# Kernel tuning notes

Hardware: AMD Instinct MI355X
Metric: run time of the kernel (lower is better)

## Reference

```python
import jax, jax.numpy as jnp
import numpy as np

B, S, D, H = 2, 2048, 2048, 16
NEG = -1e9


def setup_inputs() -> dict:
    key = jax.random.key(0)
    ks = jax.random.split(key, 5)
    x = jax.random.normal(ks[0], (B, S, D), dtype=jnp.float32)
    # additive causal mask: 0 on/below diagonal, -1e9 above
    causal = jnp.triu(jnp.full((S, S), NEG, dtype=jnp.float32), k=1)
    attn_mask = causal[None, None, :, :]  # [1,1,S,S]
    scale = 0.02
    Wq = jax.random.normal(ks[1], (D, D), dtype=jnp.float32) * scale
    Wk = jax.random.normal(ks[2], (D, D), dtype=jnp.float32) * scale
    Wv = jax.random.normal(ks[3], (D, D), dtype=jnp.float32) * scale
    Wo = jax.random.normal(ks[4], (D, D), dtype=jnp.float32) * scale
    return {"x": x, "attn_mask": attn_mask, "Wq": Wq, "Wk": Wk, "Wv": Wv, "Wo": Wo}


def reference(x, attn_mask, Wq, Wk, Wv, Wo):
    b, s, hidden = x.shape
    d = hidden // H
    # torch nn.Linear: y = x @ W.T (no bias since bias=None)
    q = (x @ Wq.T).reshape(b, s, H, d).transpose(0, 2, 1, 3)  # [b,h,s,d]
    k = (x @ Wk.T).reshape(b, s, H, d).transpose(0, 2, 1, 3)
    v = (x @ Wv.T).reshape(b, s, H, d).transpose(0, 2, 1, 3)
    q = q * (1.0 / float(d) ** 0.5)
    att = jnp.einsum("bhqd,bhkd->bhqk", q, k) + attn_mask  # [b,h,s,s]
    att = jax.nn.softmax(att.astype(jnp.float32), axis=-1).astype(x.dtype)
    y = jnp.einsum("bhqk,bhkd->bhqd", att, v)
    y = y.transpose(0, 2, 1, 3).reshape(b, s, hidden)
    return y @ Wo.T
```

## Files before the change

kernel.cpp:

```cpp
#include <hip/hip_runtime.h>
#include <hip/hip_bf16.h>
#include <cstdint>
#include <cstddef>

typedef __bf16 bf16;
typedef __bf16 bf16x8 __attribute__((ext_vector_type(8)));
typedef __bf16 bf16x4 __attribute__((ext_vector_type(4)));
typedef float f32x4 __attribute__((ext_vector_type(4)));

static constexpr int BATCH = 2;
static constexpr int SEQ = 2048;
static constexpr int DMODEL = 2048;
static constexpr int NH = 16;
static constexpr int HD = 128;
static constexpr int MROWS = BATCH * SEQ;

#define GLOBAL_AS(p) ((const __attribute__((address_space(1))) void*)(p))
#define LDS_AS(p)    ((__attribute__((address_space(3))) void*)(p))

__global__ void cvt5_kernel(const float* __restrict__ x,
                            const float* __restrict__ wq, const float* __restrict__ wk,
                            const float* __restrict__ wv, const float* __restrict__ wo,
                            bf16* __restrict__ dst) {
  const int i = blockIdx.x * blockDim.x + threadIdx.x;
  const float* src;
  int local;
  if (i < 2097152) { src = x; local = i; }
  else {
    const int r = i - 2097152;
    const int w = r >> 20;
    local = r & 1048575;
    src = (w == 0) ? wq : (w == 1) ? wk : (w == 2) ? wv : wo;
  }
  float4 f = reinterpret_cast<const float4*>(src)[local];
  bf16x4 o;
  o.x = (bf16)f.x; o.y = (bf16)f.y; o.z = (bf16)f.z; o.w = (bf16)f.w;
  reinterpret_cast<bf16x4*>(dst)[i] = o;
}

enum { MODE_QKV = 0, MODE_OUT = 1 };

template <int MODE>
__global__ __launch_bounds__(256, 4) void gemm_bt(
    const bf16* __restrict__ A, const bf16* __restrict__ W,
    bf16* __restrict__ Oq, bf16* __restrict__ Ok, bf16* __restrict__ Ov,
    float* __restrict__ Oout) {
  constexpr int Kd = DMODEL;
  __shared__ __align__(16) bf16 As[128][64];
  __shared__ __align__(16) bf16 Bs[128][64];
  const int n0 = blockIdx.x * 128;
  const int m0 = blockIdx.y * 128;
  const int tid = threadIdx.x;
  const int wave = tid >> 6;
  const int lane = tid & 63;
  const int quad = lane >> 4;
  const int l16 = lane & 15;
  const int wm = (wave >> 1) * 64;
  const int wn = (wave & 1) * 64;
  const int srow = lane >> 3;
  const int schunk = ((lane & 7) - srow) & 7;

  f32x4 acc[4][4] = {};
  for (int kt = 0; kt < Kd; kt += 64) {
#pragma unroll
    for (int i = 0; i < 4; i++) {
      const int r = wave * 32 + i * 8;
      __builtin_amdgcn_global_load_lds(
          GLOBAL_AS(&A[(size_t)(m0 + r + srow) * Kd + kt + schunk * 8]),
          LDS_AS(&As[r][0]), 16, 0, 0);
      __builtin_amdgcn_global_load_lds(
          GLOBAL_AS(&W[(size_t)(n0 + r + srow) * Kd + kt + schunk * 8]),
          LDS_AS(&Bs[r][0]), 16, 0, 0);
    }
    __syncthreads();
#pragma unroll
    for (int ks = 0; ks < 2; ks++) {
      const int col = (((ks * 4 + quad + l16) & 7)) * 8;
      bf16x8 af[4], bfr[4];
#pragma unroll
      for (int t = 0; t < 4; t++)
        af[t] = *reinterpret_cast<const bf16x8*>(&As[wm + t * 16 + l16][col]);
#pragma unroll
      for (int t = 0; t < 4; t++)
        bfr[t] = *reinterpret_cast<const bf16x8*>(&Bs[wn + t * 16 + l16][col]);
#pragma unroll
      for (int tm = 0; tm < 4; tm++)
#pragma unroll
        for (int tn = 0; tn < 4; tn++)
          acc[tm][tn] = __builtin_amdgcn_mfma_f32_16x16x32_bf16(af[tm], bfr[tn], acc[tm][tn], 0, 0, 0);
    }
    __syncthreads();
  }
#pragma unroll
  for (int tm = 0; tm < 4; tm++) {
#pragma unroll
    for (int tn = 0; tn < 4; tn++) {
      const int row0 = m0 + wm + tm * 16 + quad * 4;
      if constexpr (MODE == MODE_OUT) {
        const int col = n0 + wn + tn * 16 + l16;
#pragma unroll
        for (int j = 0; j < 4; j++)
          Oout[(size_t)(row0 + j) * DMODEL + col] = acc[tm][tn][j];
      } else {
        const int mat = n0 >> 11;
        const int col = (n0 & 2047) + wn + tn * 16 + l16;
        const int h = col >> 7, dd = col & 127;
        if (mat == 2) {
          const int b = row0 >> 11, s = row0 & 2047;
          bf16x4 pk;
#pragma unroll
          for (int j = 0; j < 4; j++) pk[j] = (bf16)acc[tm][tn][j];
          *reinterpret_cast<bf16x4*>(&Ov[((size_t)(b * NH + h) * HD + dd) * SEQ + s]) = pk;
        } else {
          bf16* O = mat ? Ok : Oq;
          const float scale = mat ? 1.0f : 0.08838834764831845f;
#pragma unroll
          for (int j = 0; j < 4; j++) {
            const int row = row0 + j;
            const int b = row >> 11, s = row & 2047;
            O[((size_t)(b * NH + h) * SEQ + s) * HD + dd] = (bf16)(acc[tm][tn][j] * scale);
          }
        }
      }
    }
  }
}

__global__ __launch_bounds__(256, 2) void attn_kernel(
    const bf16* __restrict__ Q, const bf16* __restrict__ K,
    const bf16* __restrict__ Vt, bf16* __restrict__ Y) {
  const int j = blockIdx.x;
  const int bh = blockIdx.y;
  __shared__ __align__(16) char smem[74752];
  auto Ks0 = (bf16(*)[128])(smem);
  auto Ks1 = (bf16(*)[128])(smem + 16384);
  auto Vt0 = (bf16(*)[64])(smem + 32768);
  auto Vt1 = (bf16(*)[64])(smem + 49152);
  auto Ps  = (bf16(*)[16][72])(smem + 65536);
  const int tid = threadIdx.x;
  const int wave = tid >> 6;
  const int lane = tid & 63;
  const int quad = lane >> 4;
  const int l16 = lane & 15;

  const bf16* Kbh = K + (size_t)bh * SEQ * HD;
  const bf16* Vbh = Vt + (size_t)bh * HD * SEQ;
  const int b = bh >> 4, h = bh & 15;

  const int krow = lane >> 4;
  const int vrow = lane >> 3;
  const int vchunk = ((lane & 7) - vrow) & 7;

  auto stageK = [&](int kt, bf16 (*Kd)[128]) {
#pragma unroll
    for (int i = 0; i < 4; i++) {
      const int rbase = wave * 16 + i * 4;
      const int r = rbase + krow;
      const int c = ((lane & 15) - krow - i * 4) & 15;
      __builtin_amdgcn_global_load_lds(
          GLOBAL_AS(&Kbh[(size_t)(kt + r) * HD + c * 8]), LDS_AS(&Kd[rbase][0]), 16, 0, 0);
    }
  };
  auto stageV = [&](int kt, bf16 (*Vd)[64]) {
#pragma unroll
    for (int i = 0; i < 4; i++) {
      const int rbase = wave * 32 + i * 8;
      const int r = rbase + vrow;
      __builtin_amdgcn_global_load_lds(
          GLOBAL_AS(&Vbh[(size_t)r * SEQ + kt + vchunk * 8]), LDS_AS(&Vd[rbase][0]), 16, 0, 0);
    }
  };

  for (int pass = 0; pass < 2; ++pass) {
    const int qt = pass ? (31 - j) : j;
    const int q0 = qt * 64;
    const int ntiles = qt + 1;

    const bf16* Qw = Q + ((size_t)bh * SEQ + q0 + wave * 16) * HD;
    bf16x8 qf[4];
#pragma unroll
    for (int kk = 0; kk < 4; kk++)
      qf[kk] = *reinterpret_cast<const bf16x8*>(&Qw[(size_t)l16 * HD + kk * 32 + quad * 8]);

    f32x4 oacc[8] = {};
    float m_i = -3.0e38f, l_i = 0.f;

    stageK(0, Ks0);
    stageV(0, Vt0);
    asm volatile("s_waitcnt vmcnt(0)" ::: "memory");
    __builtin_amdgcn_s_barrier();
    __builtin_amdgcn_sched_barrier(0);

    for (int t = 0; t < ntiles; ++t) {
      bf16 (*Ksc)[128] = (t & 1) ? Ks1 : Ks0;
      bf16 (*Vtc)[64]  = (t & 1) ? Vt1 : Vt0;
      if (t + 1 < ntiles) {
        bf16 (*Ksn)[128] = (t & 1) ? Ks0 : Ks1;
        bf16 (*Vtn)[64]  = (t & 1) ? Vt0 : Vt1;
        stageK((t + 1) * 64, Ksn);
        stageV((t + 1) * 64, Vtn);
      }

      f32x4 sacc[4] = {};
#pragma unroll
      for (int kk = 0; kk < 4; kk++) {
        const int kcol = (((kk * 4 + quad + l16) & 15)) * 8;
        bf16x8 ka[4];
#pragma unroll
        for (int mt = 0; mt < 4; mt++)
          ka[mt] = *reinterpret_cast<const bf16x8*>(&Ksc[mt * 16 + l16][kcol]);
#pragma unroll
        for (int mt = 0; mt < 4; mt++)
          sacc[mt] = __builtin_amdgcn_mfma_f32_16x16x32_bf16(ka[mt], qf[kk], sacc[mt], 0, 0, 0);
      }

      const int qg_loc = wave * 16 + l16;
      float mx = -3.0e38f;
      if (t == ntiles - 1) {
#pragma unroll
        for (int mt = 0; mt < 4; mt++)
#pragma unroll
          for (int jj = 0; jj < 4; jj++) {
            const int kg = mt * 16 + quad * 4 + jj;
            float v = (kg <= qg_loc) ? sacc[mt][jj] : -3.0e38f;
            sacc[mt][jj] = v;
            mx = fmaxf(mx, v);
          }
      } else {
#pragma unroll
        for (int mt = 0; mt < 4; mt++)
#pragma unroll
          for (int jj = 0; jj < 4; jj++) mx = fmaxf(mx, sacc[mt][jj]);
      }
      mx = fmaxf(mx, __shfl_xor(mx, 16));
      mx = fmaxf(mx, __shfl_xor(mx, 32));
      const float mnew = fmaxf(m_i, mx);
      const float alpha = __expf(m_i - mnew);
      m_i = mnew;
      float rs = 0.f;
#pragma unroll
      for (int mt = 0; mt < 4; mt++)
#pragma unroll
        for (int jj = 0; jj < 4; jj++) {
          float p = __expf(sacc[mt][jj] - mnew);
          sacc[mt][jj] = p;
          rs += p;
        }
      rs += __shfl_xor(rs, 16);
      rs += __shfl_xor(rs, 32);
      l_i = l_i * alpha + rs;
#pragma unroll
      for (int mt8 = 0; mt8 < 8; mt8++)
#pragma unroll
        for (int jj = 0; jj < 4; jj++) oacc[mt8][jj] *= alpha;

#pragma unroll
      for (int mt = 0; mt < 4; mt++) {
        bf16x4 pk;
#pragma unroll
        for (int jj = 0; jj < 4; jj++) pk[jj] = (bf16)sacc[mt][jj];
        *reinterpret_cast<bf16x4*>(&Ps[wave][l16][mt * 16 + quad * 4]) = pk;
      }

#pragma unroll
      for (int kk2 = 0; kk2 < 2; kk2++) {
        const int vcol = ((kk2 * 4 + quad + l16) & 7) * 8;
        bf16x8 pb = *reinterpret_cast<const bf16x8*>(&Ps[wave][l16][kk2 * 32 + quad * 8]);
#pragma unroll
        for (int mt8 = 0; mt8 < 8; mt8++) {
          bf16x8 av = *reinterpret_cast<const bf16x8*>(&Vtc[mt8 * 16 + l16][vcol]);
          oacc[mt8] = __builtin_amdgcn_mfma_f32_16x16x32_bf16(av, pb, oacc[mt8], 0, 0, 0);
        }
      }

      asm volatile("s_waitcnt vmcnt(0)" ::: "memory");
      __builtin_amdgcn_s_barrier();
      __builtin_amdgcn_sched_barrier(0);
    }

    const float inv = 1.0f / l_i;
    const int qg = q0 + wave * 16 + l16;
#pragma unroll
    for (int mt8 = 0; mt8 < 8; mt8++) {
      bf16x4 pk;
#pragma unroll
      for (int jj = 0; jj < 4; jj++) pk[jj] = (bf16)(oacc[mt8][jj] * inv);
      *reinterpret_cast<bf16x4*>(
          &Y[(size_t)(b * SEQ + qg) * DMODEL + h * HD + mt8 * 16 + quad * 4]) = pk;
    }
  }
}

extern "C" void kernel_launch(void* const* d_in, const int* in_sizes, int n_in,
                              void* d_out, int out_size, void* d_ws, size_t ws_size,
                              hipStream_t stream) {
  const float* x  = (const float*)d_in[0];
  const float* Wq = (const float*)d_in[2];
  const float* Wk = (const float*)d_in[3];
  const float* Wv = (const float*)d_in[4];
  const float* Wo = (const float*)d_in[5];
  float* out = (float*)d_out;

  char* ws = (char*)d_ws;
  bf16* xb  = (bf16*)(ws + 0);
  bf16* Wqb = (bf16*)(ws + 16777216);
  bf16* Wob = (bf16*)(ws + 41943040);
  bf16* Qb  = (bf16*)(ws + 50331648);
  bf16* Kb  = (bf16*)(ws + 67108864);
  bf16* Vtb = (bf16*)(ws + 83886080);
  bf16* Yb  = xb;
  if (ws_size < 100663296) return;

  cvt5_kernel<<<24576, 256, 0, stream>>>(x, Wq, Wk, Wv, Wo, xb);

  gemm_bt<MODE_QKV><<<dim3(48, MROWS / 128), 256, 0, stream>>>(
      xb, Wqb, Qb, Kb, Vtb, nullptr);

  attn_kernel<<<dim3(16, BATCH * NH), 256, 0, stream>>>(Qb, Kb, Vtb, Yb);

  gemm_bt<MODE_OUT><<<dim3(16, MROWS / 128), 256, 0, stream>>>(
      Yb, Wob, nullptr, nullptr, nullptr, out);
}
```

Before: 357.7 us.

## Process two 64-row query subtiles per block sharing staged K/V tiles

Each attention block now owns one 128-row query strip, split into two 64-row subtiles with separate online-softmax state. Every K/V tile staged into LDS is used by both subtiles, which halves global-to-LDS staging and the barriers per unit of work. The old scheme gave each block two 64-row passes (j and 31-j) to balance causal work. The new scheme drops that pairing and instead reverses the strip order for half the batch-heads. The cost is double the accumulator registers and unequal work per block, ranging from 2 to 32 key tiles.

After: 367.9 us. 1.03x slower.

```diff
diff --git a/kernel.cpp b/kernel.cpp
--- a/kernel.cpp
+++ b/kernel.cpp
@@ -129,8 +129,11 @@
 __global__ __launch_bounds__(256, 2) void attn_kernel(
     const bf16* __restrict__ Q, const bf16* __restrict__ K,
     const bf16* __restrict__ Vt, bf16* __restrict__ Y) {
-  const int j = blockIdx.x;
+  const int xblk = blockIdx.x;
   const int bh = blockIdx.y;
+  const int st = (bh & 16) ? (15 - xblk) : xblk;
+  const int q0 = st * 128;
+  const int ntiles = 2 * st + 2;
   __shared__ __align__(16) char smem[74752];
   auto Ks0 = (bf16(*)[128])(smem);
   auto Ks1 = (bf16(*)[128])(smem + 16384);
@@ -171,35 +174,39 @@
     }
   };
 
-  for (int pass = 0; pass < 2; ++pass) {
-    const int qt = pass ? (31 - j) : j;
-    const int q0 = qt * 64;
-    const int ntiles = qt + 1;
-
-    const bf16* Qw = Q + ((size_t)bh * SEQ + q0 + wave * 16) * HD;
-    bf16x8 qf[4];
+  bf16x8 qf[2][4];
+#pragma unroll
+  for (int s = 0; s < 2; s++) {
+    const bf16* Qw = Q + ((size_t)bh * SEQ + q0 + s * 64 + wave * 16) * HD;
 #pragma unroll
     for (int kk = 0; kk < 4; kk++)
-      qf[kk] = *reinterpret_cast<const bf16x8*>(&Qw[(size_t)l16 * HD + kk * 32 + quad * 8]);
-
-    f32x4 oacc[8] = {};
-    float m_i = -3.0e38f, l_i = 0.f;
-
-    stageK(0, Ks0);
-    stageV(0, Vt0);
-    asm volatile("s_waitcnt vmcnt(0)" ::: "memory");
-    __builtin_amdgcn_s_barrier();
-    __builtin_amdgcn_sched_barrier(0);
-
-    for (int t = 0; t < ntiles; ++t) {
-      bf16 (*Ksc)[128] = (t & 1) ? Ks1 : Ks0;
-      bf16 (*Vtc)[64]  = (t & 1) ? Vt1 : Vt0;
-      if (t + 1 < ntiles) {
-        bf16 (*Ksn)[128] = (t & 1) ? Ks0 : Ks1;
-        bf16 (*Vtn)[64]  = (t & 1) ? Vt0 : Vt1;
-        stageK((t + 1) * 64, Ksn);
-        stageV((t + 1) * 64, Vtn);
-      }
+      qf[s][kk] = *reinterpret_cast<const bf16x8*>(&Qw[(size_t)l16 * HD + kk * 32 + quad * 8]);
+  }
+
+  f32x4 oacc[2][8] = {};
+  float m_i[2] = {-3.0e38f, -3.0e38f};
+  float l_i[2] = {0.f, 0.f};
+
+  stageK(0, Ks0);
+  stageV(0, Vt0);
+  asm volatile("s_waitcnt vmcnt(0)" ::: "memory");
+  __builtin_amdgcn_s_barrier();
+  __builtin_amdgcn_sched_barrier(0);
+
+  for (int t = 0; t < ntiles; ++t) {
+    bf16 (*Ksc)[128] = (t & 1) ? Ks1 : Ks0;
+    bf16 (*Vtc)[64]  = (t & 1) ? Vt1 : Vt0;
+    if (t + 1 < ntiles) {
+      bf16 (*Ksn)[128] = (t & 1) ? Ks0 : Ks1;
+      bf16 (*Vtn)[64]  = (t & 1) ? Vt0 : Vt1;
+      stageK((t + 1) * 64, Ksn);
+      stageV((t + 1) * 64, Vtn);
+    }
+
+#pragma unroll
+    for (int s = 0; s < 2; s++) {
+      if (t > 2 * st + s) continue;
+      const bool diag = (t == 2 * st + s);
 
       f32x4 sacc[4] = {};
 #pragma unroll
@@ -211,12 +218,12 @@
           ka[mt] = *reinterpret_cast<const bf16x8*>(&Ksc[mt * 16 + l16][kcol]);
 #pragma unroll
         for (int mt = 0; mt < 4; mt++)
-          sacc[mt] = __builtin_amdgcn_mfma_f32_16x16x32_bf16(ka[mt], qf[kk], sacc[mt], 0, 0, 0);
+          sacc[mt] = __builtin_amdgcn_mfma_f32_16x16x32_bf16(ka[mt], qf[s][kk], sacc[mt], 0, 0, 0);
       }
 
       const int qg_loc = wave * 16 + l16;
       float mx = -3.0e38f;
-      if (t == ntiles - 1) {
+      if (diag) {
 #pragma unroll
         for (int mt = 0; mt < 4; mt++)
 #pragma unroll
@@ -234,9 +241,9 @@
       }
       mx = fmaxf(mx, __shfl_xor(mx, 16));
       mx = fmaxf(mx, __shfl_xor(mx, 32));
-      const float mnew = fmaxf(m_i, mx);
-      const float alpha = __expf(m_i - mnew);
-      m_i = mnew;
+      const float mnew = fmaxf(m_i[s], mx);
+      const float alpha = __expf(m_i[s] - mnew);
+      m_i[s] = mnew;
       float rs = 0.f;
 #pragma unroll
       for (int mt = 0; mt < 4; mt++)
@@ -248,11 +255,11 @@
         }
       rs += __shfl_xor(rs, 16);
       rs += __shfl_xor(rs, 32);
-      l_i = l_i * alpha + rs;
+      l_i[s] = l_i[s] * alpha + rs;
 #pragma unroll
       for (int mt8 = 0; mt8 < 8; mt8++)
 #pragma unroll
-        for (int jj = 0; jj < 4; jj++) oacc[mt8][jj] *= alpha;
+        for (int jj = 0; jj < 4; jj++) oacc[s][mt8][jj] *= alpha;
 
 #pragma unroll
       for (int mt = 0; mt < 4; mt++) {
@@ -269,22 +276,25 @@
 #pragma unroll
         for (int mt8 = 0; mt8 < 8; mt8++) {
           bf16x8 av = *reinterpret_cast<const bf16x8*>(&Vtc[mt8 * 16 + l16][vcol]);
-          oacc[mt8] = __builtin_amdgcn_mfma_f32_16x16x32_bf16(av, pb, oacc[mt8], 0, 0, 0);
+          oacc[s][mt8] = __builtin_amdgcn_mfma_f32_16x16x32_bf16(av, pb, oacc[s][mt8], 0, 0, 0);
         }
       }
-
-      asm volatile("s_waitcnt vmcnt(0)" ::: "memory");
-      __builtin_amdgcn_s_barrier();
-      __builtin_amdgcn_sched_barrier(0);
-    }
-
-    const float inv = 1.0f / l_i;
-    const int qg = q0 + wave * 16 + l16;
+    }
+
+    asm volatile("s_waitcnt vmcnt(0)" ::: "memory");
+    __builtin_amdgcn_s_barrier();
+    __builtin_amdgcn_sched_barrier(0);
+  }
+
+#pragma unroll
+  for (int s = 0; s < 2; s++) {
+    const float inv = 1.0f / l_i[s];
+    const int qg = q0 + s * 64 + wave * 16 + l16;
 #pragma unroll
     for (int mt8 = 0; mt8 < 8; mt8++) {
       bf16x4 pk;
 #pragma unroll
-      for (int jj = 0; jj < 4; jj++) pk[jj] = (bf16)(oacc[mt8][jj] * inv);
+      for (int jj = 0; jj < 4; jj++) pk[jj] = (bf16)(oacc[s][mt8][jj] * inv);
       *reinterpret_cast<bf16x4*>(
           &Y[(size_t)(b * SEQ + qg) * DMODEL + h * HD + mt8 * 16 + quad * 4]) = pk;
     }
```

## Add triple-buffered 128x256 QKV GEMM with async LDS loads

Applied to the files above, without the earlier changes.

Replaces the templated QKV projection GEMM with a dedicated kernel. It uses 512-thread blocks and 128x256 tiles, loads global memory straight into LDS, and triple-buffers shared memory so loads run two k-tiles ahead of compute. It also raises wave priority around the MFMA section. The aim is to hide global-load latency and halve the number of blocks reading A, at the cost of 144KB LDS per block, which limits occupancy. The output GEMM is split out unchanged.

Measured after the change: 371.6 us. +3.9%, slower.

```diff
diff --git a/kernel.cpp b/kernel.cpp
--- a/kernel.cpp
+++ b/kernel.cpp
@@ -38,12 +38,113 @@
   reinterpret_cast<bf16x4*>(dst)[i] = o;
 }
 
-enum { MODE_QKV = 0, MODE_OUT = 1 };
-
-template <int MODE>
-__global__ __launch_bounds__(256, 4) void gemm_bt(
+__global__ __launch_bounds__(512, 2) void gemm_qkv3(
     const bf16* __restrict__ A, const bf16* __restrict__ W,
-    bf16* __restrict__ Oq, bf16* __restrict__ Ok, bf16* __restrict__ Ov,
+    bf16* __restrict__ Oq, bf16* __restrict__ Ok, bf16* __restrict__ Ov) {
+  constexpr int Kd = DMODEL;
+  __shared__ __align__(16) char smem[147456];
+  const int n0 = blockIdx.x * 256;
+  const int m0 = blockIdx.y * 128;
+  const int tid = threadIdx.x;
+  const int wave = tid >> 6;
+  const int lane = tid & 63;
+  const int quad = lane >> 4;
+  const int l16 = lane & 15;
+  const int wm = (wave >> 2) * 64;
+  const int wn = (wave & 3) * 64;
+  const int srow = lane >> 3;
+  const int schunk = ((lane & 7) - srow) & 7;
+
+  auto stage = [&](int kt, char* base) {
+    bf16 (*As)[64] = (bf16(*)[64])base;
+    bf16 (*Bs)[64] = (bf16(*)[64])(base + 16384);
+#pragma unroll
+    for (int i = 0; i < 2; i++) {
+      const int r = wave * 16 + i * 8;
+      __builtin_amdgcn_global_load_lds(
+          GLOBAL_AS(&A[(size_t)(m0 + r + srow) * Kd + kt + schunk * 8]),
+          LDS_AS(&As[r][0]), 16, 0, 0);
+    }
+#pragma unroll
+    for (int i = 0; i < 4; i++) {
+      const int r = wave * 32 + i * 8;
+      __builtin_amdgcn_global_load_lds(
+          GLOBAL_AS(&W[(size_t)(n0 + r + srow) * Kd + kt + schunk * 8]),
+          LDS_AS(&Bs[r][0]), 16, 0, 0);
+    }
+  };
+
+  f32x4 acc[4][4] = {};
+
+  stage(0, smem);
+  stage(64, smem + 49152);
+  asm volatile("s_waitcnt vmcnt(6)" ::: "memory");
+  __builtin_amdgcn_s_barrier();
+  __builtin_amdgcn_sched_barrier(0);
+
+  int cur = 0, nxt = 1, fut = 2;
+  for (int t = 0; t < 32; ++t) {
+    if (t < 30) stage((t + 2) * 64, smem + fut * 49152);
+
+    char* cb = smem + cur * 49152;
+    bf16 (*Asc)[64] = (bf16(*)[64])cb;
+    bf16 (*Bsc)[64] = (bf16(*)[64])(cb + 16384);
+    __builtin_amdgcn_s_setprio(1);
+#pragma unroll
+    for (int ks = 0; ks < 2; ks++) {
+      const int col = (((ks * 4 + quad + l16) & 7)) * 8;
+      bf16x8 af[4], bfr[4];
+#pragma unroll
+      for (int u = 0; u < 4; u++)
+        af[u] = *reinterpret_cast<const bf16x8*>(&Asc[wm + u * 16 + l16][col]);
+#pragma unroll
+      for (int u = 0; u < 4; u++)
+        bfr[u] = *reinterpret_cast<const bf16x8*>(&Bsc[wn + u * 16 + l16][col]);
+#pragma unroll
+      for (int tm = 0; tm < 4; tm++)
+#pragma unroll
+        for (int tn = 0; tn < 4; tn++)
+          acc[tm][tn] = __builtin_amdgcn_mfma_f32_16x16x32_bf16(af[tm], bfr[tn], acc[tm][tn], 0, 0, 0);
+    }
+    __builtin_amdgcn_s_setprio(0);
+
+    if (t < 30)       { asm volatile("s_waitcnt vmcnt(6)" ::: "memory"); }
+    else if (t == 30) { asm volatile("s_waitcnt vmcnt(0)" ::: "memory"); }
+    __builtin_amdgcn_s_barrier();
+    __builtin_amdgcn_sched_barrier(0);
+    const int tmp = cur; cur = nxt; nxt = fut; fut = tmp;
+  }
+
+#pragma unroll
+  for (int tm = 0; tm < 4; tm++) {
+#pragma unroll
+    for (int tn = 0; tn < 4; tn++) {
+      const int row0 = m0 + wm + tm * 16 + quad * 4;
+      const int mat = n0 >> 11;
+      const int col = (n0 & 2047) + wn + tn * 16 + l16;
+      const int h = col >> 7, dd = col & 127;
+      if (mat == 2) {
+        const int b = row0 >> 11, s = row0 & 2047;
+        bf16x4 pk;
+#pragma unroll
+        for (int j = 0; j < 4; j++) pk[j] = (bf16)acc[tm][tn][j];
+        *reinterpret_cast<bf16x4*>(&Ov[((size_t)(b * NH + h) * HD + dd) * SEQ + s]) = pk;
+      } else {
+        bf16* O = mat ? Ok : Oq;
+        const float scale = mat ? 1.0f : 0.08838834764831845f;
+#pragma unroll
+        for (int j = 0; j < 4; j++) {
+          const int row = row0 + j;
+          const int b = row >> 11, s = row & 2047;
+          O[((size_t)(b * NH + h) * SEQ + s) * HD + dd] = (bf16)(acc[tm][tn][j] * scale);
+        }
+      }
+    }
+  }
+}
+
+__global__ __launch_bounds__(256, 4) void gemm_out(
+    const bf16* __restrict__ A, const bf16* __restrict__ W,
     float* __restrict__ Oout) {
   constexpr int Kd = DMODEL;
   __shared__ __align__(16) bf16 As[128][64];
@@ -96,32 +197,10 @@
 #pragma unroll
     for (int tn = 0; tn < 4; tn++) {
       const int row0 = m0 + wm + tm * 16 + quad * 4;
-      if constexpr (MODE == MODE_OUT) {
-        const int col = n0 + wn + tn * 16 + l16;
-#pragma unroll
-        for (int j = 0; j < 4; j++)
-          Oout[(size_t)(row0 + j) * DMODEL + col] = acc[tm][tn][j];
-      } else {
-        const int mat = n0 >> 11;
-        const int col = (n0 & 2047) + wn + tn * 16 + l16;
-        const int h = col >> 7, dd = col & 127;
-        if (mat == 2) {
-          const int b = row0 >> 11, s = row0 & 2047;
-          bf16x4 pk;
-#pragma unroll
-          for (int j = 0; j < 4; j++) pk[j] = (bf16)acc[tm][tn][j];
-          *reinterpret_cast<bf16x4*>(&Ov[((size_t)(b * NH + h) * HD + dd) * SEQ + s]) = pk;
-        } else {
-          bf16* O = mat ? Ok : Oq;
-          const float scale = mat ? 1.0f : 0.08838834764831845f;
-#pragma unroll
-          for (int j = 0; j < 4; j++) {
-            const int row = row0 + j;
-            const int b = row >> 11, s = row & 2047;
-            O[((size_t)(b * NH + h) * SEQ + s) * HD + dd] = (bf16)(acc[tm][tn][j] * scale);
-          }
-        }
-      }
+      const int col = n0 + wn + tn * 16 + l16;
+#pragma unroll
+      for (int j = 0; j < 4; j++)
+        Oout[(size_t)(row0 + j) * DMODEL + col] = acc[tm][tn][j];
     }
   }
 }
@@ -313,11 +392,11 @@
 
   cvt5_kernel<<<24576, 256, 0, stream>>>(x, Wq, Wk, Wv, Wo, xb);
 
-  gemm_bt<MODE_QKV><<<dim3(48, MROWS / 128), 256, 0, stream>>>(
-      xb, Wqb, Qb, Kb, Vtb, nullptr);
+  gemm_qkv3<<<dim3(24, MROWS / 128), 512, 0, stream>>>(
+      xb, Wqb, Qb, Kb, Vtb);
 
   attn_kernel<<<dim3(16, BATCH * NH), 256, 0, stream>>>(Qb, Kb, Vtb, Yb);
 
-  gemm_bt<MODE_OUT><<<dim3(16, MROWS / 128), 256, 0, stream>>>(
-      Yb, Wob, nullptr, nullptr, nullptr, out);
+  gemm_out<<<dim3(16, MROWS / 128), 256, 0, stream>>>(
+      Yb, Wob, out);
 }
```
